# Kernel tuning notes

Hardware: AMD Instinct MI355X
Metric: run time of the kernel (lower is better)

## Reference

```python
import jax, jax.numpy as jnp
import numpy as np

NUM_HEADS = 16
FOCUS_FACTOR = 1.6
HEAD_REGION = {0: 0, 1: 1, 2: 2}  # head -> region (first/middle/end)


def setup_inputs() -> dict:
    key = jax.random.key(0)
    k1, k2, k3, k4, k5 = jax.random.split(key, 5)
    B, S, D = 2, 2048, 1024
    # GPT-2 style init scale so softmax is not fully saturated
    return {
        "hidden_states": jax.random.normal(k1, (B, S, D), dtype=jnp.float32),
        "c_attn_w": jax.random.normal(k2, (D, 3 * D), dtype=jnp.float32) * 0.02,
        "c_attn_b": jax.random.normal(k3, (3 * D,), dtype=jnp.float32) * 0.02,
        "c_proj_w": jax.random.normal(k4, (D, D), dtype=jnp.float32) * 0.02,
        "c_proj_b": jax.random.normal(k5, (D,), dtype=jnp.float32) * 0.02,
    }


def _region_multipliers(seq_len: int, num_heads: int, factor: float) -> jnp.ndarray:
    """[H, S] multiplier: selected heads up-weight their token region."""
    first_end = max(1, seq_len // 3)
    second_end = max(first_end + 1, 2 * seq_len // 3)
    pos = jnp.arange(seq_len)
    regions = [
        pos < first_end,
        (pos >= first_end) & (pos < second_end),
        pos >= second_end,
    ]
    mult = np.ones((num_heads, seq_len), dtype=np.float32)
    mult = jnp.asarray(mult)
    for h, r in HEAD_REGION.items():
        if h < num_heads:
            mult = mult.at[h].set(1.0 + (factor - 1.0) * regions[r].astype(jnp.float32))
    return mult


def reference(hidden_states, c_attn_w, c_attn_b, c_proj_w, c_proj_b):
    B, S, D = hidden_states.shape
    H = NUM_HEADS
    hd = D // H

    qkv = hidden_states @ c_attn_w + c_attn_b  # [B, S, 3D]
    q, k, v = jnp.split(qkv, 3, axis=-1)

    def _reshape(x):  # [B, S, D] -> [B, H, S, hd]
        return x.reshape(B, S, H, hd).transpose(0, 2, 1, 3)

    q, k, v = _reshape(q), _reshape(k), _reshape(v)

    scores = jnp.einsum("bhqd,bhkd->bhqk", q, k) / jnp.sqrt(jnp.float32(hd))
    causal = jnp.tril(jnp.ones((S, S), dtype=bool))
    mask_value = jnp.finfo(scores.dtype).min
    scores = jnp.where(causal[None, None], scores, mask_value)

    attn = jax.nn.softmax(scores, axis=-1)  # [B, H, S, S]

    # Per-head region reweight + renorm (only for the divergent heads)
    mult = _region_multipliers(S, H, FOCUS_FACTOR)  # [H, S]
    scaled = attn * mult[None, :, None, :]
    scaled = scaled / jnp.sum(scaled, axis=-1, keepdims=True)
    div_heads = jnp.zeros((H,), dtype=bool)
    for h in HEAD_REGION:
        if h < H:
            div_heads = div_heads.at[h].set(True)
    attn = jnp.where(div_heads[None, :, None, None], scaled, attn)

    out = jnp.einsum("bhqk,bhkd->bhqd", attn, v)  # [B, H, S, hd]
    out = out.transpose(0, 2, 1, 3).reshape(B, S, D)
    out = out @ c_proj_w + c_proj_b
    return out
```

## Files before the change

### kernel.cpp

```cpp
#include <hip/hip_runtime.h>
#include <hip/hip_bf16.h>

typedef __attribute__((ext_vector_type(8))) short bf16x8;
typedef __attribute__((ext_vector_type(4))) float f32x4;
typedef __attribute__((ext_vector_type(16))) float f32x16;
typedef __attribute__((ext_vector_type(4))) unsigned int u32x4;
typedef unsigned short u16;

#define MFMA_BF16(a, b, c) __builtin_amdgcn_mfma_f32_16x16x32_bf16(a, b, c, 0, 0, 0)
#define MFMA32(a, b, c) __builtin_amdgcn_mfma_f32_32x32x16_bf16(a, b, c, 0, 0, 0)

__device__ inline u16 f2b(float x) {
  unsigned int u = __builtin_bit_cast(unsigned int, x);
  u += 0x7fffu + ((u >> 16) & 1u);
  return (u16)(u >> 16);
}

__device__ inline float exp2_fast(float x) {
  float r;
  asm("v_exp_f32 %0, %1" : "=v"(r) : "v"(x));
  return r;
}

__device__ inline unsigned int cvtpk_bf16(float lo, float hi) {
  unsigned int r;
  asm("v_cvt_pk_bf16_f32 %0, %1, %2" : "=v"(r) : "v"(lo), "v"(hi));
  return r;
}

__device__ inline void pswap(unsigned int& dst, unsigned int& src) {
  asm("v_permlane32_swap_b32 %0, %1" : "+v"(dst), "+v"(src));
}

__device__ inline void gload16(void* lds, const void* g) {
  __builtin_amdgcn_global_load_lds((const __attribute__((address_space(1))) void*)g,
                                   (__attribute__((address_space(3))) void*)lds,
                                   16, 0, 0);
}


__global__ __launch_bounds__(256) void cast_f32_bf16(const float* __restrict__ src,
                                                     u16* __restrict__ dst, int n4) {
  int i = blockIdx.x * blockDim.x + threadIdx.x;
  if (i < n4) {
    float4 v = ((const float4*)src)[i];
    ushort4 o;
    o.x = f2b(v.x); o.y = f2b(v.y); o.z = f2b(v.z); o.w = f2b(v.w);
    ((ushort4*)dst)[i] = o;
  }
}

__global__ __launch_bounds__(256) void transpose_cast(const float* __restrict__ src,
                                                      u16* __restrict__ dst, int K, int N) {
  __shared__ float t[32][33];
  int k0 = blockIdx.x * 32, n0 = blockIdx.y * 32;
  int tx = threadIdx.x, ty = threadIdx.y;
#pragma unroll
  for (int i = 0; i < 4; i++) t[ty + i * 8][tx] = src[(size_t)(k0 + ty + i * 8) * N + n0 + tx];
  __syncthreads();
#pragma unroll
  for (int i = 0; i < 4; i++)
    dst[(size_t)(n0 + ty + i * 8) * K + k0 + tx] = f2b(t[tx][ty + i * 8]);
}

#define QSCALE 0.1803368801f

__global__ __launch_bounds__(512, 2) void gemm256_qkv(
    const u16* __restrict__ A, const u16* __restrict__ BT, const float* __restrict__ bias,
    u16* __restrict__ oQ, u16* __restrict__ oK, u16* __restrict__ oVf) {
  __shared__ __align__(16) u16 As[2][256 * 64];
  __shared__ __align__(16) u16 Bs[2][256 * 64];
  const int K = 1024, NT = 16;
  int tid = threadIdx.x;
  int wv = tid >> 6, lane = tid & 63, lr = lane & 15, lg = lane >> 4;
  int wm = wv >> 2, wn = wv & 3;
  int bx = blockIdx.x % 12, by = blockIdx.x / 12;
  int m0 = by * 256, n0 = bx * 256;
  const int swz = (lr & 7) << 4;

  f32x4 acc[8][4] = {};

  auto stageA = [&](int buf, int kt, int h) {
#pragma unroll
    for (int g = 0; g < 2; g++) {
      int li = g * 512 + tid;
      int row = (li >> 3) + h * 128;
      int cb = ((li & 7) * 16) ^ ((row & 7) << 4);
      gload16((char*)&As[buf][0] + h * 16384 + g * 8192 + wv * 1024,
              (const char*)(A + (size_t)(m0 + row) * K + kt * 64) + cb);
    }
  };
  auto stageB = [&](int buf, int kt, int h) {
#pragma unroll
    for (int g = 0; g < 2; g++) {
      int li = g * 512 + tid;
      int row = (li >> 3) + h * 128;
      int cb = ((li & 7) * 16) ^ ((row & 7) << 4);
      gload16((char*)&Bs[buf][0] + h * 16384 + g * 8192 + wv * 1024,
              (const char*)(BT + (size_t)(n0 + row) * K + kt * 64) + cb);
    }
  };

  stageA(0, 0, 0);
  stageB(0, 0, 0);
  stageA(0, 0, 1);
  stageB(0, 0, 1);

  for (int t = 0; t < NT; ++t) {
    const int buf = t & 1;
    const bool last = (t == NT - 1);
#pragma unroll
    for (int p = 0; p < 4; p++) {
      const int Mq = p & 1, Nq = p >> 1;
      if (last) {
        if (p == 0) asm volatile("s_waitcnt vmcnt(0)" ::: "memory");
      } else if (p < 3) {
        asm volatile("s_waitcnt vmcnt(4)" ::: "memory");
      }
      __builtin_amdgcn_s_barrier();
      bf16x8 a[4][2], b[2][2];
#pragma unroll
      for (int ii = 0; ii < 4; ii++) {
        int row = wm * 16 + ii * 32 + Mq * 128 + lr;
#pragma unroll
        for (int kk = 0; kk < 2; kk++)
          a[ii][kk] = *(const bf16x8*)((const char*)&As[buf][0] + row * 128 +
                                       ((kk * 64 + lg * 16) ^ swz));
      }
#pragma unroll
      for (int jj2 = 0; jj2 < 2; jj2++) {
        int row = wn * 16 + jj2 * 64 + Nq * 128 + lr;
#pragma unroll
        for (int kk = 0; kk < 2; kk++)
          b[jj2][kk] = *(const bf16x8*)((const char*)&Bs[buf][0] + row * 128 +
                                        ((kk * 64 + lg * 16) ^ swz));
      }
      if (!last) {
        if (p == 0) stageA(buf ^ 1, t + 1, 0);
        else if (p == 1) stageB(buf ^ 1, t + 1, 0);
        else if (p == 2) stageA(buf ^ 1, t + 1, 1);
        else stageB(buf ^ 1, t + 1, 1);
      }
      __builtin_amdgcn_s_setprio(1);
#pragma unroll
      for (int ii = 0; ii < 4; ii++)
#pragma unroll
        for (int jj2 = 0; jj2 < 2; jj2++)
#pragma unroll
          for (int kk = 0; kk < 2; kk++)
            acc[Mq * 4 + ii][Nq * 2 + jj2] =
                MFMA_BF16(a[ii][kk], b[jj2][kk], acc[Mq * 4 + ii][Nq * 2 + jj2]);
      __builtin_amdgcn_s_setprio(0);
    }
  }

#pragma unroll
  for (int i = 0; i < 8; i++) {
#pragma unroll
    for (int j = 0; j < 4; j++) {
#pragma unroll
      for (int jj = 0; jj < 4; jj++) {
        int row = m0 + wm * 16 + (i & 3) * 32 + (i >> 2) * 128 + lg * 4 + jj;
        int col = n0 + wn * 16 + (j & 1) * 64 + (j >> 1) * 128 + lr;
        float v = acc[i][j][jj] + bias[col];
        int bb = row >> 11, s = row & 2047;
        int tile = s >> 6, key = s & 63;
        if (col < 1024) {
          oQ[((size_t)((bb * 16 + (col >> 6)) * 2048 + s)) * 64 + (col & 63)] = f2b(v * QSCALE);
        } else if (col < 2048) {
          int c = col - 1024;
          int hh = c >> 6, d = c & 63;
          int jf = ((key >> 5) << 2) + (d >> 4);
          int ln = (((d >> 3) & 1) << 5) | (key & 31);
          oK[(size_t)(bb * 16 + hh) * 131072 + tile * 4096 + jf * 512 + ln * 8 + (d & 7)] =
              f2b(v);
        } else {
          int c = col - 2048;
          int hh = c >> 6, d = c & 63;
          int jf = ((d >> 5) << 2) + (key >> 4);
          int ln = (((key >> 3) & 1) << 5) | (d & 31);
          oVf[(size_t)(bb * 16 + hh) * 131072 + tile * 4096 + jf * 512 + ln * 8 + (key & 7)] =
              f2b(v);
        }
      }
    }
  }
}

__global__ __launch_bounds__(256) void gemm_bt_f32(
    const u16* __restrict__ A, const u16* __restrict__ BT, const float* __restrict__ bias,
    float* __restrict__ oF, int M, int N, int K, int nbx) {
  __shared__ __align__(16) u16 As[128 * 64];
  __shared__ __align__(16) u16 Bs[128 * 64];
  int tid = threadIdx.x;
  int wv = tid >> 6, lane = tid & 63, lr = lane & 15, lg = lane >> 4;
  int bx = blockIdx.x % nbx, by = blockIdx.x / nbx;
  int m0 = by * 128, n0 = bx * 128;
  int wr = (wv >> 1) * 64, wc = (wv & 1) * 64;

  f32x4 acc[4][4] = {};

  for (int k0 = 0; k0 < K; k0 += 64) {
#pragma unroll
    for (int j = 0; j < 4; j++) {
      int li = j * 256 + tid;
      int row = li >> 3;
      int cb = ((li & 7) * 16) ^ ((row & 7) << 4);
      gload16((char*)As + j * 4096 + wv * 1024,
              (const char*)(A + (size_t)(m0 + row) * K + k0) + cb);
      gload16((char*)Bs + j * 4096 + wv * 1024,
              (const char*)(BT + (size_t)(n0 + row) * K + k0) + cb);
    }
    __syncthreads();
#pragma unroll
    for (int kk = 0; kk < 2; kk++) {
      bf16x8 a[4], b[4];
#pragma unroll
      for (int i = 0; i < 4; i++) {
        int row = wr + i * 16 + lr;
        a[i] = *(const bf16x8*)((const char*)As + row * 128 +
                                ((kk * 64 + lg * 16) ^ ((row & 7) << 4)));
      }
#pragma unroll
      for (int j = 0; j < 4; j++) {
        int row = wc + j * 16 + lr;
        b[j] = *(const bf16x8*)((const char*)Bs + row * 128 +
                                ((kk * 64 + lg * 16) ^ ((row & 7) << 4)));
      }
#pragma unroll
      for (int i = 0; i < 4; i++)
#pragma unroll
        for (int j = 0; j < 4; j++) acc[i][j] = MFMA_BF16(a[i], b[j], acc[i][j]);
    }
    __syncthreads();
  }

#pragma unroll
  for (int i = 0; i < 4; i++)
#pragma unroll
    for (int j = 0; j < 4; j++)
#pragma unroll
      for (int jj = 0; jj < 4; jj++) {
        int row = m0 + wr + i * 16 + lg * 4 + jj;
        int col = n0 + wc + j * 16 + lr;
        oF[(size_t)row * N + col] = acc[i][j][jj] + bias[col];
      }
}

#define SEQL 2048
#define FIRST_END 682
#define SECOND_END 1365
#define LOG2F16 0.6780719051f

__global__ __launch_bounds__(256) void attn_kernel(const u16* __restrict__ Qb,
                                                   const u16* __restrict__ Kf,
                                                   const u16* __restrict__ Vf,
                                                   u16* __restrict__ AO) {
  __shared__ float Ol[4][16][66];
  __shared__ float Ml[4][32], Ll[4][32], Cl[4][32];

  int tid = threadIdx.x;
  int w = tid >> 6, l = tid & 63;
  int r31 = l & 31, hi = l >> 5;

  int xcd = blockIdx.x & 7, slot = blockIdx.x >> 3;
  int bh = xcd * 4 + (slot >> 6);
  int qt = 63 - (slot & 63);
  int q0 = qt * 32;
  int h = bh & 15, b = bh >> 4;

  const u16* Qp = Qb + ((size_t)bh * SEQL + q0 + r31) * 64 + hi * 8;
  bf16x8 qa[4];
#pragma unroll
  for (int kb = 0; kb < 4; kb++) qa[kb] = *(const bf16x8*)(Qp + kb * 16);

  const u16* Kfp = Kf + (size_t)bh * 131072;
  const u16* Vfp = Vf + (size_t)bh * 131072;

  f32x16 o0 = {}, o1 = {};
  float m = -1e30f, lsum = 0.f;

  const int N = (q0 + 95) >> 6;
  const bool hasb = (h < 3);

  for (int t = w; t < N; t += 4) {
    const int kv0 = t << 6;
    const bool last = (t == N - 1);
    const u16* kt = Kfp + (size_t)t * 4096;
    const u16* vt = Vfp + (size_t)t * 4096;

    bf16x8 ka[4], kb2[4];
#pragma unroll
    for (int kb = 0; kb < 4; kb++) {
      ka[kb]  = *(const bf16x8*)(kt + kb * 512 + l * 8);
      kb2[kb] = *(const bf16x8*)(kt + (4 + kb) * 512 + l * 8);
    }
    f32x16 sA = {}, sB = {};
#pragma unroll
    for (int kb = 0; kb < 4; kb++) sA = MFMA32(ka[kb], qa[kb], sA);
#pragma unroll
    for (int kb = 0; kb < 4; kb++) sB = MFMA32(kb2[kb], qa[kb], sB);

    if (hasb) {
#pragma unroll
      for (int r = 0; r < 16; r++) {
        int kA = kv0 + ((r & 3) + 8 * (r >> 2) + 4 * hi);
        int kB = kA + 32;
        int rA = (kA < FIRST_END) ? 0 : (kA < SECOND_END) ? 1 : 2;
        int rB = (kB < FIRST_END) ? 0 : (kB < SECOND_END) ? 1 : 2;
        if (rA == h) sA[r] += LOG2F16;
        if (rB == h) sB[r] += LOG2F16;
      }
    }
    if (last) {
      int q = q0 + r31;
#pragma unroll
      for (int r = 0; r < 16; r++) {
        int kA = kv0 + ((r & 3) + 8 * (r >> 2) + 4 * hi);
        if (kA > q) sA[r] = -1e30f;
        if (kA + 32 > q) sB[r] = -1e30f;
      }
    }

#define MAX4(v, i) fmaxf(fmaxf(v[i], v[i + 1]), fmaxf(v[i + 2], v[i + 3]))
    float mA = fmaxf(fmaxf(MAX4(sA, 0), MAX4(sA, 4)), fmaxf(MAX4(sA, 8), MAX4(sA, 12)));
    float mB = fmaxf(fmaxf(MAX4(sB, 0), MAX4(sB, 4)), fmaxf(MAX4(sB, 8), MAX4(sB, 12)));
    float mx = fmaxf(mA, mB);
    mx = fmaxf(mx, __shfl_xor(mx, 32));
    float mn = fmaxf(m, mx);
    float corr = exp2_fast(m - mn);
    m = mn;

    unsigned int wA[8], wB[8];
    float s0 = 0.f, s1 = 0.f;
#pragma unroll
    for (int i = 0; i < 8; i++) {
      float pa0 = exp2_fast(sA[2 * i] - mn), pa1 = exp2_fast(sA[2 * i + 1] - mn);
      float pb0 = exp2_fast(sB[2 * i] - mn), pb1 = exp2_fast(sB[2 * i + 1] - mn);
      s0 += pa0 + pa1;
      s1 += pb0 + pb1;
      wA[i] = cvtpk_bf16(pa0, pa1);
      wB[i] = cvtpk_bf16(pb0, pb1);
    }
    float ssum = s0 + s1;
    ssum += __shfl_xor(ssum, 32);
    lsum = lsum * corr + ssum;
    o0 *= corr;
    o1 *= corr;

    pswap(wA[0], wA[2]); pswap(wA[1], wA[3]);
    pswap(wA[4], wA[6]); pswap(wA[5], wA[7]);
    pswap(wB[0], wB[2]); pswap(wB[1], wB[3]);
    pswap(wB[4], wB[6]); pswap(wB[5], wB[7]);

    bf16x8 pb[4];
    pb[0] = __builtin_bit_cast(bf16x8, (u32x4){wA[0], wA[1], wA[2], wA[3]});
    pb[1] = __builtin_bit_cast(bf16x8, (u32x4){wA[4], wA[5], wA[6], wA[7]});
    pb[2] = __builtin_bit_cast(bf16x8, (u32x4){wB[0], wB[1], wB[2], wB[3]});
    pb[3] = __builtin_bit_cast(bf16x8, (u32x4){wB[4], wB[5], wB[6], wB[7]});

#pragma unroll
    for (int c = 0; c < 4; c++) {
      bf16x8 va0 = *(const bf16x8*)(vt + c * 512 + l * 8);
      bf16x8 va1 = *(const bf16x8*)(vt + (4 + c) * 512 + l * 8);
      o0 = MFMA32(va0, pb[c], o0);
      o1 = MFMA32(va1, pb[c], o1);
    }
  }

  Ml[w][r31] = m;
  Ll[w][r31] = lsum;
#pragma unroll
  for (int r = 0; r < 16; r++) Ol[w][r][l] = o0[r];
  __syncthreads();

  if (tid < 128) {
    int w2 = tid >> 5, q = tid & 31;
    float m0 = Ml[0][q], m1 = Ml[1][q], m2 = Ml[2][q], m3 = Ml[3][q];
    float ms = fmaxf(fmaxf(m0, m1), fmaxf(m2, m3));
    float e0 = exp2_fast(m0 - ms), e1 = exp2_fast(m1 - ms);
    float e2 = exp2_fast(m2 - ms), e3 = exp2_fast(m3 - ms);
    float ls = Ll[0][q] * e0 + Ll[1][q] * e1 + Ll[2][q] * e2 + Ll[3][q] * e3;
    float ei = (w2 == 0) ? e0 : (w2 == 1) ? e1 : (w2 == 2) ? e2 : e3;
    Cl[w2][q] = ei / ls;
  }
  __syncthreads();

  int mq = tid >> 3, md = (tid & 7) * 4;
  float c0 = Cl[0][mq], c1 = Cl[1][mq], c2 = Cl[2][mq], c3 = Cl[3][mq];
  u16* aop = AO + ((size_t)(b * SEQL + q0 + mq)) * 1024 + h * 64;

  {
    u16 ov[4];
#pragma unroll
    for (int j = 0; j < 4; j++) {
      int d = md + j;
      int h2 = (d >> 2) & 1, rr = (d & 3) + 4 * (d >> 3);
      int ll2 = mq + 32 * h2;
      ov[j] = f2b(Ol[0][rr][ll2] * c0 + Ol[1][rr][ll2] * c1 +
                  Ol[2][rr][ll2] * c2 + Ol[3][rr][ll2] * c3);
    }
    *(uint2*)(aop + md) = *(const uint2*)ov;
  }
  __syncthreads();
#pragma unroll
  for (int r = 0; r < 16; r++) Ol[w][r][l] = o1[r];
  __syncthreads();
  {
    u16 ov[4];
#pragma unroll
    for (int j = 0; j < 4; j++) {
      int d = md + j;
      int h2 = (d >> 2) & 1, rr = (d & 3) + 4 * (d >> 3);
      int ll2 = mq + 32 * h2;
      ov[j] = f2b(Ol[0][rr][ll2] * c0 + Ol[1][rr][ll2] * c1 +
                  Ol[2][rr][ll2] * c2 + Ol[3][rr][ll2] * c3);
    }
    *(uint2*)(aop + 32 + md) = *(const uint2*)ov;
  }
}


extern "C" void kernel_launch(void* const* d_in, const int* in_sizes, int n_in,
                              void* d_out, int out_size, void* d_ws, size_t ws_size,
                              hipStream_t stream) {
  const float* hs = (const float*)d_in[0];
  const float* w1 = (const float*)d_in[1];
  const float* b1 = (const float*)d_in[2];
  const float* w2 = (const float*)d_in[3];
  const float* b2 = (const float*)d_in[4];
  float* out = (float*)d_out;

  char* ws = (char*)d_ws;
  const size_t MB = 1u << 20;
  u16* hsb = (u16*)(ws + 0);
  u16* w1t = (u16*)(ws + 8 * MB);
  u16* w2t = (u16*)(ws + 14 * MB);
  u16* Qb = (u16*)(ws + 16 * MB);
  u16* Kf = (u16*)(ws + 24 * MB);
  u16* Vf = (u16*)(ws + 32 * MB);
  u16* AO = hsb;

  cast_f32_bf16<<<4096, 256, 0, stream>>>(hs, hsb, 4096 * 1024 / 4);
  dim3 tb(32, 8);
  transpose_cast<<<dim3(32, 96), tb, 0, stream>>>(w1, w1t, 1024, 3072);
  transpose_cast<<<dim3(32, 32), tb, 0, stream>>>(w2, w2t, 1024, 1024);

  gemm256_qkv<<<16 * 12, 512, 0, stream>>>(hsb, w1t, b1, Qb, Kf, Vf);
  attn_kernel<<<2048, 256, 0, stream>>>(Qb, Kf, Vf, AO);
  gemm_bt_f32<<<32 * 8, 256, 0, stream>>>(AO, w2t, b2, out, 4096, 1024, 1024, 8);
}
```

Before: 130.6 us.

## Reschedule QKV GEMM phases for fragment reuse and add lazy softmax rescaling

The QKV GEMM main loop is restructured into four explicit phases per k-tile. A and B fragments are reused across quadrants (a/b0, a/b1, a_hi/b0, a_hi/b1), which cuts LDS reads, and the global staging order and waits are adjusted to match. The attention kernel now skips the online-softmax rescale of the running sum and accumulators unless some lane's max grows by more than 8 in log2 units, in the style of FA4. It also raises wave priority around the MFMA blocks. This reduces exp and multiply work per tile, at the cost of allowing unnormalized exponentials up to 2^8, which stays safe in fp32 but could affect bf16 P precision.

```diff
diff --git a/kernel.cpp b/kernel.cpp
--- a/kernel.cpp
+++ b/kernel.cpp
@@ -76,7 +76,6 @@
   int wm = wv >> 2, wn = wv & 3;
   int bx = blockIdx.x % 12, by = blockIdx.x / 12;
   int m0 = by * 256, n0 = bx * 256;
-  const int swz = (lr & 7) << 4;
 
   f32x4 acc[8][4] = {};
 
@@ -101,57 +100,101 @@
     }
   };
 
-  stageA(0, 0, 0);
-  stageB(0, 0, 0);
-  stageA(0, 0, 1);
-  stageB(0, 0, 1);
+  stageA(0, 0, 0); stageB(0, 0, 0); stageB(0, 0, 1); stageA(0, 0, 1);
 
   for (int t = 0; t < NT; ++t) {
     const int buf = t & 1;
     const bool last = (t == NT - 1);
-#pragma unroll
-    for (int p = 0; p < 4; p++) {
-      const int Mq = p & 1, Nq = p >> 1;
-      if (last) {
-        if (p == 0) asm volatile("s_waitcnt vmcnt(0)" ::: "memory");
-      } else if (p < 3) {
-        asm volatile("s_waitcnt vmcnt(4)" ::: "memory");
-      }
-      __builtin_amdgcn_s_barrier();
-      bf16x8 a[4][2], b[2][2];
-#pragma unroll
-      for (int ii = 0; ii < 4; ii++) {
-        int row = wm * 16 + ii * 32 + Mq * 128 + lr;
+    const char* Ab = (const char*)&As[buf][0];
+    const char* Bb = (const char*)&Bs[buf][0];
+    bf16x8 a[4][2], b0[2][2], b1[2][2];
+
+    if (last) asm volatile("s_waitcnt vmcnt(0)" ::: "memory");
+    else      asm volatile("s_waitcnt vmcnt(4)" ::: "memory");
+    __builtin_amdgcn_s_barrier();
+#pragma unroll
+    for (int ii = 0; ii < 4; ii++) {
+      int row = wm * 16 + ii * 32 + lr;
+#pragma unroll
+      for (int kk = 0; kk < 2; kk++)
+        a[ii][kk] = *(const bf16x8*)(Ab + row * 128 + ((kk * 64 + lg * 16) ^ ((row & 7) << 4)));
+    }
+#pragma unroll
+    for (int jj2 = 0; jj2 < 2; jj2++) {
+      int row = wn * 16 + jj2 * 64 + lr;
+#pragma unroll
+      for (int kk = 0; kk < 2; kk++)
+        b0[jj2][kk] = *(const bf16x8*)(Bb + row * 128 + ((kk * 64 + lg * 16) ^ ((row & 7) << 4)));
+    }
+    if (!last) stageA(buf ^ 1, t + 1, 0);
+    __builtin_amdgcn_s_setprio(1);
+#pragma unroll
+    for (int ii = 0; ii < 4; ii++)
+#pragma unroll
+      for (int jj2 = 0; jj2 < 2; jj2++)
 #pragma unroll
         for (int kk = 0; kk < 2; kk++)
-          a[ii][kk] = *(const bf16x8*)((const char*)&As[buf][0] + row * 128 +
-                                       ((kk * 64 + lg * 16) ^ swz));
-      }
-#pragma unroll
-      for (int jj2 = 0; jj2 < 2; jj2++) {
-        int row = wn * 16 + jj2 * 64 + Nq * 128 + lr;
+          acc[ii][jj2] = MFMA_BF16(a[ii][kk], b0[jj2][kk], acc[ii][jj2]);
+    __builtin_amdgcn_s_setprio(0);
+    __builtin_amdgcn_sched_barrier(0);
+    __builtin_amdgcn_s_barrier();
+
+    if (!last) asm volatile("s_waitcnt vmcnt(4)" ::: "memory");
+    __builtin_amdgcn_s_barrier();
+#pragma unroll
+    for (int jj2 = 0; jj2 < 2; jj2++) {
+      int row = wn * 16 + jj2 * 64 + 128 + lr;
+#pragma unroll
+      for (int kk = 0; kk < 2; kk++)
+        b1[jj2][kk] = *(const bf16x8*)(Bb + row * 128 + ((kk * 64 + lg * 16) ^ ((row & 7) << 4)));
+    }
+    if (!last) stageB(buf ^ 1, t + 1, 0);
+    __builtin_amdgcn_s_setprio(1);
+#pragma unroll
+    for (int ii = 0; ii < 4; ii++)
+#pragma unroll
+      for (int jj2 = 0; jj2 < 2; jj2++)
 #pragma unroll
         for (int kk = 0; kk < 2; kk++)
-          b[jj2][kk] = *(const bf16x8*)((const char*)&Bs[buf][0] + row * 128 +
-                                        ((kk * 64 + lg * 16) ^ swz));
-      }
-      if (!last) {
-        if (p == 0) stageA(buf ^ 1, t + 1, 0);
-        else if (p == 1) stageB(buf ^ 1, t + 1, 0);
-        else if (p == 2) stageA(buf ^ 1, t + 1, 1);
-        else stageB(buf ^ 1, t + 1, 1);
-      }
-      __builtin_amdgcn_s_setprio(1);
-#pragma unroll
-      for (int ii = 0; ii < 4; ii++)
-#pragma unroll
-        for (int jj2 = 0; jj2 < 2; jj2++)
-#pragma unroll
-          for (int kk = 0; kk < 2; kk++)
-            acc[Mq * 4 + ii][Nq * 2 + jj2] =
-                MFMA_BF16(a[ii][kk], b[jj2][kk], acc[Mq * 4 + ii][Nq * 2 + jj2]);
-      __builtin_amdgcn_s_setprio(0);
-    }
+          acc[ii][2 + jj2] = MFMA_BF16(a[ii][kk], b1[jj2][kk], acc[ii][2 + jj2]);
+    __builtin_amdgcn_s_setprio(0);
+    __builtin_amdgcn_sched_barrier(0);
+    __builtin_amdgcn_s_barrier();
+
+    if (!last) asm volatile("s_waitcnt vmcnt(4)" ::: "memory");
+    __builtin_amdgcn_s_barrier();
+#pragma unroll
+    for (int ii = 0; ii < 4; ii++) {
+      int row = wm * 16 + ii * 32 + 128 + lr;
+#pragma unroll
+      for (int kk = 0; kk < 2; kk++)
+        a[ii][kk] = *(const bf16x8*)(Ab + row * 128 + ((kk * 64 + lg * 16) ^ ((row & 7) << 4)));
+    }
+    if (!last) stageB(buf ^ 1, t + 1, 1);
+    __builtin_amdgcn_s_setprio(1);
+#pragma unroll
+    for (int ii = 0; ii < 4; ii++)
+#pragma unroll
+      for (int jj2 = 0; jj2 < 2; jj2++)
+#pragma unroll
+        for (int kk = 0; kk < 2; kk++)
+          acc[4 + ii][jj2] = MFMA_BF16(a[ii][kk], b0[jj2][kk], acc[4 + ii][jj2]);
+    __builtin_amdgcn_s_setprio(0);
+    __builtin_amdgcn_sched_barrier(0);
+    __builtin_amdgcn_s_barrier();
+
+    if (!last) stageA(buf ^ 1, t + 1, 1);
+    __builtin_amdgcn_s_setprio(1);
+#pragma unroll
+    for (int ii = 0; ii < 4; ii++)
+#pragma unroll
+      for (int jj2 = 0; jj2 < 2; jj2++)
+#pragma unroll
+        for (int kk = 0; kk < 2; kk++)
+          acc[4 + ii][2 + jj2] = MFMA_BF16(a[ii][kk], b1[jj2][kk], acc[4 + ii][2 + jj2]);
+    __builtin_amdgcn_s_setprio(0);
+    __builtin_amdgcn_sched_barrier(0);
+    __builtin_amdgcn_s_barrier();
   }
 
 #pragma unroll
@@ -296,10 +339,12 @@
       kb2[kb] = *(const bf16x8*)(kt + (4 + kb) * 512 + l * 8);
     }
     f32x16 sA = {}, sB = {};
+    __builtin_amdgcn_s_setprio(1);
 #pragma unroll
     for (int kb = 0; kb < 4; kb++) sA = MFMA32(ka[kb], qa[kb], sA);
 #pragma unroll
     for (int kb = 0; kb < 4; kb++) sB = MFMA32(kb2[kb], qa[kb], sB);
+    __builtin_amdgcn_s_setprio(0);
 
     if (hasb) {
 #pragma unroll
@@ -327,16 +372,21 @@
     float mB = fmaxf(fmaxf(MAX4(sB, 0), MAX4(sB, 4)), fmaxf(MAX4(sB, 8), MAX4(sB, 12)));
     float mx = fmaxf(mA, mB);
     mx = fmaxf(mx, __shfl_xor(mx, 32));
-    float mn = fmaxf(m, mx);
-    float corr = exp2_fast(m - mn);
-    m = mn;
+    if (!__all(mx - m <= 8.0f)) {
+      float mn = fmaxf(m, mx);
+      float corr = exp2_fast(m - mn);
+      m = mn;
+      lsum *= corr;
+      o0 *= corr;
+      o1 *= corr;
+    }
 
     unsigned int wA[8], wB[8];
     float s0 = 0.f, s1 = 0.f;
 #pragma unroll
     for (int i = 0; i < 8; i++) {
-      float pa0 = exp2_fast(sA[2 * i] - mn), pa1 = exp2_fast(sA[2 * i + 1] - mn);
-      float pb0 = exp2_fast(sB[2 * i] - mn), pb1 = exp2_fast(sB[2 * i + 1] - mn);
+      float pa0 = exp2_fast(sA[2 * i] - m), pa1 = exp2_fast(sA[2 * i + 1] - m);
+      float pb0 = exp2_fast(sB[2 * i] - m), pb1 = exp2_fast(sB[2 * i + 1] - m);
       s0 += pa0 + pa1;
       s1 += pb0 + pb1;
       wA[i] = cvtpk_bf16(pa0, pa1);
@@ -344,9 +394,7 @@
     }
     float ssum = s0 + s1;
     ssum += __shfl_xor(ssum, 32);
-    lsum = lsum * corr + ssum;
-    o0 *= corr;
-    o1 *= corr;
+    lsum += ssum;
 
     pswap(wA[0], wA[2]); pswap(wA[1], wA[3]);
     pswap(wA[4], wA[6]); pswap(wA[5], wA[7]);
@@ -359,6 +407,7 @@
     pb[2] = __builtin_bit_cast(bf16x8, (u32x4){wB[0], wB[1], wB[2], wB[3]});
     pb[3] = __builtin_bit_cast(bf16x8, (u32x4){wB[4], wB[5], wB[6], wB[7]});
 
+    __builtin_amdgcn_s_setprio(1);
 #pragma unroll
     for (int c = 0; c < 4; c++) {
       bf16x8 va0 = *(const bf16x8*)(vt + c * 512 + l * 8);
@@ -366,6 +415,7 @@
       o0 = MFMA32(va0, pb[c], o0);
       o1 = MFMA32(va1, pb[c], o1);
     }
+    __builtin_amdgcn_s_setprio(0);
   }
 
   Ml[w][r31] = m;
```

Result: slower. 142.1 us (+8.8%).
